# Performance work log

Measured on AMD Instinct MI355X. Metric: run time of the kernel, lower is better.

## Reference

```python
import jax, jax.numpy as jnp
import numpy as np

ARITY = 4
DEPTH = 8          # leaves = ARITY**DEPTH = 65536; internal nodes = (4**8-1)//3 = 21845
IN_DIM = 64
MEM = 128
HID = 128


def setup_inputs() -> dict:
    key = jax.random.key(0)
    ks = jax.random.split(key, 20)
    n_leaves = ARITY ** DEPTH
    n_internal = (ARITY ** DEPTH - 1) // (ARITY - 1)
    s = 0.05
    inp = {
        "inputs": jax.random.normal(ks[0], (n_leaves, IN_DIM), jnp.float32),
        "ops": jax.random.randint(ks[1], (n_internal,), 0, 2, jnp.int32),
        # MLP (all bias-free); torch Linear weight layout [out, in]
        "W1": jax.random.normal(ks[2], (MEM, IN_DIM), jnp.float32) * s,
        "W2": jax.random.normal(ks[3], (3 * MEM, MEM), jnp.float32) * s,
        "W3": jax.random.normal(ks[4], (2 * MEM, 3 * MEM), jnp.float32) * s,
        "Wp": jax.random.normal(ks[5], (MEM, 2 * MEM), jnp.float32) * s,
        # ChildSumTreeRNN
        "Wand": jax.random.normal(ks[6], (MEM, MEM), jnp.float32) * s,
        "Wor": jax.random.normal(ks[7], (MEM, MEM), jnp.float32) * s,
        "Rw1": jax.random.normal(ks[8], (HID, MEM), jnp.float32) * s,
        "Rb1": jnp.zeros((HID,), jnp.float32),
        "Rw2": jax.random.normal(ks[9], (HID, HID), jnp.float32) * s,
        "Rb2": jnp.zeros((HID,), jnp.float32),
        "Rw3": jax.random.normal(ks[10], (HID, HID), jnp.float32) * s,
        "Rb3": jnp.zeros((HID,), jnp.float32),
        "Rwp": jax.random.normal(ks[11], (1, HID), jnp.float32) * s,
        "Rbp": jnp.zeros((1,), jnp.float32),
    }
    return inp


def reference(inputs, ops, W1, W2, W3, Wp, Wand, Wor,
              Rw1, Rb1, Rw2, Rb2, Rw3, Rb3, Rwp, Rbp):
    # MLP embedding of all leaves  [n_leaves, MEM]
    h = jnp.tanh(inputs @ W1.T)
    h = jnp.tanh(h @ W2.T)
    h = jnp.tanh(h @ W3.T)
    h = jnp.tanh(h @ Wp.T)

    # ChildSumTreeRNN, level by level (children before parents).
    # Complete arity-4 tree: level l has 4**l internal nodes; ops is
    # level-ordered from the root, so level l starts at (4**l - 1)//3.
    for l in range(DEPTH - 1, -1, -1):
        n = ARITY ** l
        start = (ARITY ** l - 1) // (ARITY - 1)
        ops_l = ops[start:start + n]                      # [n]
        ch = h.reshape(n, ARITY, MEM)                     # children states
        ha = jnp.tanh(jnp.einsum('ncm,om->nco', ch, Wand)).mean(axis=1)
        ho = jnp.tanh(jnp.einsum('ncm,om->nco', ch, Wor)).mean(axis=1)
        h = jnp.where((ops_l == 0)[:, None], ha, ho)      # [n, MEM]

    x = jax.nn.relu(h @ Rw1.T + Rb1)
    x = jax.nn.relu(x @ Rw2.T + Rb2)
    x = jax.nn.relu(x @ Rw3.T + Rb3)
    out = x @ Rwp.T + Rbp                                 # [1, 1]
    return out
```

## Files before the change

### kernel.cpp

```cpp
#include <hip/hip_runtime.h>
#include <hip/hip_bf16.h>
#include <stdint.h>

#define N_LEAVES 65536
#define MEM 128
#define HID 128

typedef float  f32x4 __attribute__((ext_vector_type(4)));
typedef short  s16x8 __attribute__((ext_vector_type(8)));
typedef unsigned short u16;
typedef u16    u16x8 __attribute__((ext_vector_type(8)));

__device__ __forceinline__ u16 f2bf(float x) {
    unsigned u = __builtin_bit_cast(unsigned, x);
    u += 0x7FFFu + ((u >> 16) & 1u);
    return (u16)(u >> 16);
}
__device__ __forceinline__ float bf2f(u16 b) {
    unsigned u = ((unsigned)b) << 16;
    return __builtin_bit_cast(float, u);
}
__device__ __forceinline__ float hif(float x) {
    return __builtin_bit_cast(float, __builtin_bit_cast(unsigned, x) & 0xffff0000u);
}
__device__ __forceinline__ unsigned packbf(float e0, float e1) {
    return __builtin_amdgcn_perm(__builtin_bit_cast(unsigned, e1),
                                 __builtin_bit_cast(unsigned, e0), 0x07060302u);
}
__device__ __forceinline__ float tanh_c(float x) {
    float E = __builtin_amdgcn_exp2f(x * 2.8853900817779268f);
    return 1.0f - 2.0f * __builtin_amdgcn_rcpf(E + 1.0f);
}
__device__ __forceinline__ float tanh_p(float x) {
    float x2 = x * x;
    float poly = x * (1.0f + x2 * (-0.33333334f + x2 * 0.13333334f));
    float E = __builtin_amdgcn_exp2f(x * 2.8853900817779268f);
    float ex = 1.0f - 2.0f * __builtin_amdgcn_rcpf(E + 1.0f);
    return (__builtin_fabsf(x) < 0.25f) ? poly : ex;
}

__device__ __forceinline__ f32x4 mfma_bf(s16x8 a, s16x8 b, f32x4 c) {
    return __builtin_amdgcn_mfma_f32_16x16x32_bf16(a, b, c, 0, 0, 0);
}

__global__ __launch_bounds__(256) void prep_all(
    const float* __restrict__ W1, const float* __restrict__ W2,
    const float* __restrict__ W3, const float* __restrict__ Wp,
    const float* __restrict__ Wand, const float* __restrict__ Wor,
    u16* __restrict__ w1tH, u16* __restrict__ w1tL,
    u16* __restrict__ w2tH, u16* __restrict__ w2tL,
    u16* __restrict__ w3tH, u16* __restrict__ w3tL,
    u16* __restrict__ wptH, u16* __restrict__ wptL,
    u16* __restrict__ waH,  u16* __restrict__ waL,
    u16* __restrict__ woH,  u16* __restrict__ woL)
{
    int g = blockIdx.x * 256 + threadIdx.x;
    const float* W; u16 *Th, *Tl; int K, N, base;
    if (g < 1024)       { W = W1;  Th = w1tH; Tl = w1tL; N = 128; K = 64;  base = 0; }
    else if (g < 7168)  { W = W2;  Th = w2tH; Tl = w2tL; N = 384; K = 128; base = 1024; }
    else if (g < 19456) { W = W3;  Th = w3tH; Tl = w3tL; N = 256; K = 384; base = 7168; }
    else if (g < 23552) { W = Wp;  Th = wptH; Tl = wptL; N = 128; K = 256; base = 19456; }
    else if (g < 25600) { W = Wand; Th = waH; Tl = waL;  N = 128; K = 128; base = 23552; }
    else if (g < 27648) { W = Wor;  Th = woH; Tl = woL;  N = 128; K = 128; base = 25600; }
    else return;
    int t = g - base;
    int kg8 = K >> 3;
    int n = t / kg8, kg = t - n * kg8;
    const float* src = &W[(size_t)n * K + kg * 8];
    size_t dst = ((size_t)kg * N + n) * 8;
    u16x8 hv, lv;
    #pragma unroll
    for (int j = 0; j < 8; ++j) {
        float v = src[j];
        u16 hb = f2bf(v);
        hv[j] = hb;
        lv[j] = f2bf(v - bf2f(hb));
    }
    *(u16x8*)&Th[dst] = hv;
    *(u16x8*)&Tl[dst] = lv;
}

__device__ __forceinline__ int act_g(int Wu, int row, int c4) {
    return row * (Wu >> 3) + (c4 ^ (row & 7));
}

template<int FJ, int KTN, int WIN, int WOUT>
__device__ __forceinline__ void mlp_layer_t(
    const u16* inH, const u16* inL,
    const u16* __restrict__ BtH, const u16* __restrict__ BtL,
    u16* outH, u16* outL,
    int w, int l)
{
    const int lr = l & 15, lc = l >> 4;
    const int featBase = w * (FJ * 16);
    constexpr int D = (KTN < 3) ? KTN : 3;

    f32x4 acc[FJ][4] = {};
    s16x8 wh[D][FJ], wl[D][FJ];
    s16x8 ah[2][4], al[2][4];

    #pragma unroll
    for (int d = 0; d < D; ++d)
        #pragma unroll
        for (int fi = 0; fi < FJ; ++fi) {
            int o = ((d * 4 + lc) * WOUT + featBase + fi * 16 + lr) * 8;
            wh[d][fi] = *(const s16x8*)&BtH[o];
            wl[d][fi] = *(const s16x8*)&BtL[o];
        }
    #pragma unroll
    for (int rj = 0; rj < 4; ++rj) {
        int off = act_g(WIN, rj * 16 + lr, lc) * 8;
        ah[0][rj] = *(const s16x8*)&inH[off];
        al[0][rj] = *(const s16x8*)&inL[off];
    }

    #pragma unroll
    for (int kt = 0; kt < KTN; ++kt) {
        const int ws_ = kt % D;
        const int as_ = kt & 1;
        if (kt + 1 < KTN) {
            #pragma unroll
            for (int rj = 0; rj < 4; ++rj) {
                int off = act_g(WIN, rj * 16 + lr, (kt + 1) * 4 + lc) * 8;
                ah[as_ ^ 1][rj] = *(const s16x8*)&inH[off];
                al[as_ ^ 1][rj] = *(const s16x8*)&inL[off];
            }
        }
        #pragma unroll
        for (int fi = 0; fi < FJ; ++fi)
            #pragma unroll
            for (int rj = 0; rj < 4; ++rj) {
                f32x4 a = acc[fi][rj];
                a = mfma_bf(wh[ws_][fi], ah[as_][rj], a);
                a = mfma_bf(wh[ws_][fi], al[as_][rj], a);
                a = mfma_bf(wl[ws_][fi], ah[as_][rj], a);
                acc[fi][rj] = a;
            }
        if (kt + D < KTN) {
            #pragma unroll
            for (int fi = 0; fi < FJ; ++fi) {
                int o = (((kt + D) * 4 + lc) * WOUT + featBase + fi * 16 + lr) * 8;
                wh[ws_][fi] = *(const s16x8*)&BtH[o];
                wl[ws_][fi] = *(const s16x8*)&BtL[o];
            }
        }
    }

    #pragma unroll
    for (int fi = 0; fi < FJ; ++fi)
        #pragma unroll
        for (int rj = 0; rj < 4; ++rj) {
            int m  = rj * 16 + lr;
            int n0 = featBase + fi * 16 + lc * 4;
            f32x4 v = acc[fi][rj];
            float t0 = tanh_c(v[0]), t1 = tanh_c(v[1]);
            float t2 = tanh_c(v[2]), t3 = tanh_c(v[3]);
            uint2 hp, lp;
            hp.x = packbf(t0, t1);
            hp.y = packbf(t2, t3);
            lp.x = packbf(t0 - hif(t0), t1 - hif(t1));
            lp.y = packbf(t2 - hif(t2), t3 - hif(t3));
            int go = act_g(WOUT, m, n0 >> 3) * 8 + (n0 & 7);
            *(uint2*)&outH[go] = hp;
            *(uint2*)&outL[go] = lp;
        }
}

template<int CJ, int FJ, bool TOGLOBAL>
__device__ __forceinline__ void tree_level(
    const u16* inH, const u16* inL,
    const u16* __restrict__ wAH, const u16* __restrict__ wAL,
    const u16* __restrict__ wOH, const u16* __restrict__ wOL,
    const int* __restrict__ opsL,
    u16* outH, u16* outL,
    int outRowBase, int nValid, int cfBase, int ffBase, int l)
{
    const int lr = l & 15, lc = l >> 4;
    f32x4 accA[CJ][FJ] = {};
    f32x4 accO[CJ][FJ] = {};

    #pragma unroll
    for (int kt = 0; kt < 4; ++kt) {
        s16x8 ah[CJ], al[CJ];
        #pragma unroll
        for (int c = 0; c < CJ; ++c) {
            int off = act_g(128, (cfBase + c) * 16 + lr, kt * 4 + lc) * 8;
            ah[c] = *(const s16x8*)&inH[off];
            al[c] = *(const s16x8*)&inL[off];
        }
        #pragma unroll
        for (int f = 0; f < FJ; ++f) {
            int wo = ((kt * 4 + lc) * 128 + ffBase + f * 16 + lr) * 8;
            s16x8 bah = *(const s16x8*)&wAH[wo];
            s16x8 bal = *(const s16x8*)&wAL[wo];
            s16x8 boh = *(const s16x8*)&wOH[wo];
            s16x8 bol = *(const s16x8*)&wOL[wo];
            #pragma unroll
            for (int c = 0; c < CJ; ++c) {
                f32x4 a = accA[c][f];
                a = mfma_bf(ah[c], bah, a);
                a = mfma_bf(ah[c], bal, a);
                a = mfma_bf(al[c], bah, a);
                accA[c][f] = a;
                f32x4 o = accO[c][f];
                o = mfma_bf(ah[c], boh, o);
                o = mfma_bf(ah[c], bol, o);
                o = mfma_bf(al[c], boh, o);
                accO[c][f] = o;
            }
        }
    }

    #pragma unroll
    for (int c = 0; c < CJ; ++c) {
        int p = (cfBase + c) * 4 + lc;
        if (p < nValid) {
            int op = opsL[p];
            #pragma unroll
            for (int f = 0; f < FJ; ++f) {
                f32x4 v = op ? accO[c][f] : accA[c][f];
                float t = 0.25f * (tanh_p(v[0]) + tanh_p(v[1]) + tanh_p(v[2]) + tanh_p(v[3]));
                unsigned bits = __builtin_bit_cast(unsigned, t);
                u16 hb = (u16)(bits >> 16);
                float lof = t - __builtin_bit_cast(float, bits & 0xffff0000u);
                u16 lb = (u16)(__builtin_bit_cast(unsigned, lof) >> 16);
                int feat = ffBase + f * 16 + lr;
                if constexpr (TOGLOBAL) {
                    int ga = (outRowBase + p) * 128 + feat;
                    outH[ga] = hb;
                    outL[ga] = lb;
                } else {
                    int go = act_g(128, outRowBase + p, feat >> 3) * 8 + (feat & 7);
                    outH[go] = hb;
                    outL[go] = lb;
                }
            }
        }
    }
}

__global__ __launch_bounds__(512, 1) void leaf_fused(
    const float* __restrict__ x,
    const u16* __restrict__ W1tH, const u16* __restrict__ W1tL,
    const u16* __restrict__ W2tH, const u16* __restrict__ W2tL,
    const u16* __restrict__ W3tH, const u16* __restrict__ W3tL,
    const u16* __restrict__ WptH, const u16* __restrict__ WptL,
    const u16* __restrict__ waH,  const u16* __restrict__ waL,
    const u16* __restrict__ woH,  const u16* __restrict__ woL,
    const int* __restrict__ ops,
    u16* __restrict__ l7H, u16* __restrict__ l7L)
{
    __shared__ u16 bufA[49152];
    __shared__ u16 bufB[32768];

    const int tid = threadIdx.x;
    const int w = tid >> 6, l = tid & 63;
    const int blk = blockIdx.x;
    const int rowBase = blk * 64;

    {
        int row = tid >> 3;
        int c0  = (tid & 7) * 8;
        const float* src = &x[(size_t)(rowBase + row) * 64 + c0];
        float4 v0 = *(const float4*)src;
        float4 v1 = *(const float4*)(src + 4);
        float xs[8] = {v0.x, v0.y, v0.z, v0.w, v1.x, v1.y, v1.z, v1.w};
        int go = act_g(64, row, c0 >> 3) * 8;
        uint4 hp, lp;
        hp.x = packbf(xs[0], xs[1]); hp.y = packbf(xs[2], xs[3]);
        hp.z = packbf(xs[4], xs[5]); hp.w = packbf(xs[6], xs[7]);
        lp.x = packbf(xs[0] - hif(xs[0]), xs[1] - hif(xs[1]));
        lp.y = packbf(xs[2] - hif(xs[2]), xs[3] - hif(xs[3]));
        lp.z = packbf(xs[4] - hif(xs[4]), xs[5] - hif(xs[5]));
        lp.w = packbf(xs[6] - hif(xs[6]), xs[7] - hif(xs[7]));
        *(uint4*)&bufB[go] = hp;
        *(uint4*)&bufB[4096 + go] = lp;
    }
    __syncthreads();

    mlp_layer_t<1, 2, 64, 128>(bufB, bufB + 4096, W1tH, W1tL,
                               bufB + 8192, bufB + 16384, w, l);
    __syncthreads();
    mlp_layer_t<3, 4, 128, 384>(bufB + 8192, bufB + 16384, W2tH, W2tL,
                                bufA, bufA + 24576, w, l);
    __syncthreads();
    mlp_layer_t<2, 12, 384, 256>(bufA, bufA + 24576, W3tH, W3tL,
                                 bufB, bufB + 16384, w, l);
    __syncthreads();
    mlp_layer_t<1, 8, 256, 128>(bufB, bufB + 16384, WptH, WptL,
                                bufA, bufA + 8192, w, l);
    __syncthreads();
    tree_level<1, 4, true>(bufA, bufA + 8192, waH, waL, woH, woL,
                           ops + 5461 + blk * 16, l7H, l7L,
                           blk * 16, 16, (w >> 1), (w & 1) * 64, l);
}

__global__ __launch_bounds__(512, 4) void tree3(
    const u16* __restrict__ inH, const u16* __restrict__ inL,
    const u16* __restrict__ wAH, const u16* __restrict__ wAL,
    const u16* __restrict__ wOH, const u16* __restrict__ wOL,
    const int* __restrict__ ops0, const int* __restrict__ ops1,
    const int* __restrict__ ops2,
    u16* __restrict__ outH, u16* __restrict__ outL)
{
    __shared__ u16 L0H[16384], L0L[16384];
    __shared__ u16 L1H[4096],  L1L[4096];

    const int tid = threadIdx.x;
    const int w = tid >> 6, l = tid & 63;
    const int blk = blockIdx.x;

    #pragma unroll
    for (int it = 0; it < 4; ++it) {
        int g = tid + it * 512;
        int row = g >> 4, c4 = g & 15;
        size_t src = (size_t)(blk * 128 + row) * 128 + c4 * 8;
        int dst = act_g(128, row, c4) * 8;
        *(u16x8*)&L0H[dst] = *(const u16x8*)&inH[src];
        *(u16x8*)&L0L[dst] = *(const u16x8*)&inL[src];
    }
    __syncthreads();

    tree_level<2, 4, false>(L0H, L0L, wAH, wAL, wOH, wOL, ops0 + blk * 32,
                            L1H, L1L, 0, 32, (w & 3) * 2, (w >> 2) * 64, l);
    __syncthreads();
    tree_level<1, 2, false>(L1H, L1L, wAH, wAL, wOH, wOL, ops1 + blk * 8,
                            L0H, L0L, 0, 8, (w >> 2), (w & 3) * 32, l);
    __syncthreads();
    tree_level<1, 1, true>(L0H, L0L, wAH, wAL, wOH, wOL, ops2 + blk * 2,
                           outH, outL, blk * 2, 2, 0, w * 16, l);
}

__global__ __launch_bounds__(128) void tail_final(
    const u16* __restrict__ l1H, const u16* __restrict__ l1L,
    const int* __restrict__ ops,
    const float* __restrict__ Wand, const float* __restrict__ Wor,
    const float* __restrict__ Rw1, const float* __restrict__ Rb1,
    const float* __restrict__ Rw2, const float* __restrict__ Rb2,
    const float* __restrict__ Rw3, const float* __restrict__ Rb3,
    const float* __restrict__ Rwp, const float* __restrict__ Rbp,
    float* __restrict__ out)
{
    __shared__ float h[512];
    __shared__ float F[512];
    const int o = threadIdx.x;

    for (int i = o; i < 512; i += 128) h[i] = bf2f(l1H[i]) + bf2f(l1L[i]);
    __syncthreads();

    {
        const float* Wsel = (ops[0] == 0) ? Wand : Wor;
        const float4* wr = (const float4*)&Wsel[o * 128];
        const float4* h0 = (const float4*)&h[0];
        const float4* h1 = (const float4*)&h[128];
        const float4* h2 = (const float4*)&h[256];
        const float4* h3 = (const float4*)&h[384];
        float s0 = 0, s1 = 0, s2 = 0, s3 = 0;
        for (int m = 0; m < 32; ++m) {
            float4 wv = wr[m];
            float4 a0 = h0[m], a1 = h1[m], a2 = h2[m], a3 = h3[m];
            s0 += wv.x*a0.x + wv.y*a0.y + wv.z*a0.z + wv.w*a0.w;
            s1 += wv.x*a1.x + wv.y*a1.y + wv.z*a1.z + wv.w*a1.w;
            s2 += wv.x*a2.x + wv.y*a2.y + wv.z*a2.z + wv.w*a2.w;
            s3 += wv.x*a3.x + wv.y*a3.y + wv.z*a3.z + wv.w*a3.w;
        }
        F[o] = 0.25f * (tanh_p(s0) + tanh_p(s1) + tanh_p(s2) + tanh_p(s3));
    }
    __syncthreads();
    {
        const float4* wr = (const float4*)&Rw1[o * 128];
        const float4* xr = (const float4*)&F[0];
        float s = 0;
        for (int m = 0; m < 32; ++m) {
            float4 wv = wr[m], xv = xr[m];
            s += wv.x*xv.x + wv.y*xv.y + wv.z*xv.z + wv.w*xv.w;
        }
        __syncthreads();
        F[128 + o] = fmaxf(s + Rb1[o], 0.f);
    }
    __syncthreads();
    {
        const float4* wr = (const float4*)&Rw2[o * 128];
        const float4* xr = (const float4*)&F[128];
        float s = 0;
        for (int m = 0; m < 32; ++m) {
            float4 wv = wr[m], xv = xr[m];
            s += wv.x*xv.x + wv.y*xv.y + wv.z*xv.z + wv.w*xv.w;
        }
        __syncthreads();
        F[256 + o] = fmaxf(s + Rb2[o], 0.f);
    }
    __syncthreads();
    {
        const float4* wr = (const float4*)&Rw3[o * 128];
        const float4* xr = (const float4*)&F[256];
        float s = 0;
        for (int m = 0; m < 32; ++m) {
            float4 wv = wr[m], xv = xr[m];
            s += wv.x*xv.x + wv.y*xv.y + wv.z*xv.z + wv.w*xv.w;
        }
        __syncthreads();
        F[384 + o] = fmaxf(s + Rb3[o], 0.f) * Rwp[o];
    }
    __syncthreads();
    if (o == 0) {
        float t = 0.f;
        for (int i = 0; i < 128; ++i) t += F[384 + i];
        out[0] = t + Rbp[0];
    }
}

extern "C" void kernel_launch(void* const* d_in, const int* in_sizes, int n_in,
                              void* d_out, int out_size, void* d_ws, size_t ws_size,
                              hipStream_t stream)
{
    const float* inputs = (const float*)d_in[0];
    const int*   ops    = (const int*)d_in[1];
    const float* W1     = (const float*)d_in[2];
    const float* W2     = (const float*)d_in[3];
    const float* W3     = (const float*)d_in[4];
    const float* Wp     = (const float*)d_in[5];
    const float* Wand   = (const float*)d_in[6];
    const float* Wor    = (const float*)d_in[7];
    const float* Rw1    = (const float*)d_in[8];
    const float* Rb1    = (const float*)d_in[9];
    const float* Rw2    = (const float*)d_in[10];
    const float* Rb2    = (const float*)d_in[11];
    const float* Rw3    = (const float*)d_in[12];
    const float* Rb3    = (const float*)d_in[13];
    const float* Rwp    = (const float*)d_in[14];
    const float* Rbp    = (const float*)d_in[15];
    float* out = (float*)d_out;
    u16* ws = (u16*)d_ws;

    size_t off = 0;
    u16* w1tH = ws + off; off += 8192;   u16* w1tL = ws + off; off += 8192;
    u16* w2tH = ws + off; off += 49152;  u16* w2tL = ws + off; off += 49152;
    u16* w3tH = ws + off; off += 98304;  u16* w3tL = ws + off; off += 98304;
    u16* wptH = ws + off; off += 32768;  u16* wptL = ws + off; off += 32768;
    u16* waH  = ws + off; off += 16384;  u16* waL  = ws + off; off += 16384;
    u16* woH  = ws + off; off += 16384;  u16* woL  = ws + off; off += 16384;
    u16* l7H  = ws + off; off += (size_t)16384 * 128;
    u16* l7L  = ws + off; off += (size_t)16384 * 128;
    u16* l4H  = ws + off; off += 256 * 128;
    u16* l4L  = ws + off; off += 256 * 128;
    u16* l1H  = ws + off; off += 512;
    u16* l1L  = ws + off; off += 512;

    prep_all<<<108, 256, 0, stream>>>(W1, W2, W3, Wp, Wand, Wor,
        w1tH, w1tL, w2tH, w2tL, w3tH, w3tL, wptH, wptL, waH, waL, woH, woL);

    leaf_fused<<<N_LEAVES / 64, 512, 0, stream>>>(
        inputs, w1tH, w1tL, w2tH, w2tL, w3tH, w3tL, wptH, wptL,
        waH, waL, woH, woL, ops, l7H, l7L);

    tree3<<<128, 512, 0, stream>>>(l7H, l7L, waH, waL, woH, woL,
        ops + 1365, ops + 341, ops + 85, l4H, l4L);

    tree3<<<2, 512, 0, stream>>>(l4H, l4L, waH, waL, woH, woL,
        ops + 21, ops + 5, ops + 1, l1H, l1L);

    tail_final<<<1, 128, 0, stream>>>(l1H, l1L, ops, Wand, Wor,
        Rw1, Rb1, Rw2, Rb2, Rw3, Rb3, Rwp, Rbp, out);
}
```

Measured before the change: 143.0 us.

## Chunk W2/W3 layers to shrink LDS footprint and raise leaf kernel occupancy

The fused leaf MLP kernel now computes the 384-wide hidden layer in three 128-wide chunks, each immediately consumed by a partial K-slice of the W3 layer, so the full 384-wide activation never sits in shared memory. LDS drops from two buffers (~160KB) to one 64KB pool with aliased regions, and launch bounds go from 1 to 4 blocks per CU. The MFMA inner loop is restructured to double-buffer weights and load activations per row tile instead of double-buffering activations. This adds extra barriers and register pressure from the 4-block bound, but aims to hide latency through more resident waves.

```diff
diff --git a/kernel.cpp b/kernel.cpp
--- a/kernel.cpp
+++ b/kernel.cpp
@@ -84,68 +84,56 @@
     return row * (Wu >> 3) + (c4 ^ (row & 7));
 }
 
-template<int FJ, int KTN, int WIN, int WOUT>
-__device__ __forceinline__ void mlp_layer_t(
+template<int FJ, int KTN, int WINU, int WSTR>
+__device__ __forceinline__ void mlp_core(
+    f32x4 (&acc)[FJ][4],
     const u16* inH, const u16* inL,
     const u16* __restrict__ BtH, const u16* __restrict__ BtL,
-    u16* outH, u16* outL,
-    int w, int l)
+    int kt0, int featBase, int l)
 {
     const int lr = l & 15, lc = l >> 4;
-    const int featBase = w * (FJ * 16);
-    constexpr int D = (KTN < 3) ? KTN : 3;
-
-    f32x4 acc[FJ][4] = {};
-    s16x8 wh[D][FJ], wl[D][FJ];
-    s16x8 ah[2][4], al[2][4];
-
-    #pragma unroll
-    for (int d = 0; d < D; ++d)
-        #pragma unroll
-        for (int fi = 0; fi < FJ; ++fi) {
-            int o = ((d * 4 + lc) * WOUT + featBase + fi * 16 + lr) * 8;
-            wh[d][fi] = *(const s16x8*)&BtH[o];
-            wl[d][fi] = *(const s16x8*)&BtL[o];
-        }
-    #pragma unroll
-    for (int rj = 0; rj < 4; ++rj) {
-        int off = act_g(WIN, rj * 16 + lr, lc) * 8;
-        ah[0][rj] = *(const s16x8*)&inH[off];
-        al[0][rj] = *(const s16x8*)&inL[off];
+    s16x8 wh[2][FJ], wl[2][FJ];
+
+    #pragma unroll
+    for (int fi = 0; fi < FJ; ++fi) {
+        int o = ((kt0 * 4 + lc) * WSTR + featBase + fi * 16 + lr) * 8;
+        wh[0][fi] = *(const s16x8*)&BtH[o];
+        wl[0][fi] = *(const s16x8*)&BtL[o];
     }
 
     #pragma unroll
     for (int kt = 0; kt < KTN; ++kt) {
-        const int ws_ = kt % D;
-        const int as_ = kt & 1;
+        const int cur = kt & 1;
         if (kt + 1 < KTN) {
             #pragma unroll
-            for (int rj = 0; rj < 4; ++rj) {
-                int off = act_g(WIN, rj * 16 + lr, (kt + 1) * 4 + lc) * 8;
-                ah[as_ ^ 1][rj] = *(const s16x8*)&inH[off];
-                al[as_ ^ 1][rj] = *(const s16x8*)&inL[off];
+            for (int fi = 0; fi < FJ; ++fi) {
+                int o = (((kt0 + kt + 1) * 4 + lc) * WSTR + featBase + fi * 16 + lr) * 8;
+                wh[cur ^ 1][fi] = *(const s16x8*)&BtH[o];
+                wl[cur ^ 1][fi] = *(const s16x8*)&BtL[o];
             }
         }
         #pragma unroll
-        for (int fi = 0; fi < FJ; ++fi)
+        for (int rj = 0; rj < 4; ++rj) {
+            int off = act_g(WINU, rj * 16 + lr, kt * 4 + lc) * 8;
+            s16x8 ah = *(const s16x8*)&inH[off];
+            s16x8 al = *(const s16x8*)&inL[off];
             #pragma unroll
-            for (int rj = 0; rj < 4; ++rj) {
+            for (int fi = 0; fi < FJ; ++fi) {
                 f32x4 a = acc[fi][rj];
-                a = mfma_bf(wh[ws_][fi], ah[as_][rj], a);
-                a = mfma_bf(wh[ws_][fi], al[as_][rj], a);
-                a = mfma_bf(wl[ws_][fi], ah[as_][rj], a);
+                a = mfma_bf(wh[cur][fi], ah, a);
+                a = mfma_bf(wh[cur][fi], al, a);
+                a = mfma_bf(wl[cur][fi], ah, a);
                 acc[fi][rj] = a;
             }
-        if (kt + D < KTN) {
-            #pragma unroll
-            for (int fi = 0; fi < FJ; ++fi) {
-                int o = (((kt + D) * 4 + lc) * WOUT + featBase + fi * 16 + lr) * 8;
-                wh[ws_][fi] = *(const s16x8*)&BtH[o];
-                wl[ws_][fi] = *(const s16x8*)&BtL[o];
-            }
-        }
-    }
-
+        }
+    }
+}
+
+template<int FJ, int WOUTU>
+__device__ __forceinline__ void write_act(
+    f32x4 (&acc)[FJ][4], u16* outH, u16* outL, int featBase, int l)
+{
+    const int lr = l & 15, lc = l >> 4;
     #pragma unroll
     for (int fi = 0; fi < FJ; ++fi)
         #pragma unroll
@@ -160,7 +148,7 @@
             hp.y = packbf(t2, t3);
             lp.x = packbf(t0 - hif(t0), t1 - hif(t1));
             lp.y = packbf(t2 - hif(t2), t3 - hif(t3));
-            int go = act_g(WOUT, m, n0 >> 3) * 8 + (n0 & 7);
+            int go = act_g(WOUTU, m, n0 >> 3) * 8 + (n0 & 7);
             *(uint2*)&outH[go] = hp;
             *(uint2*)&outL[go] = lp;
         }
@@ -239,7 +227,7 @@
     }
 }
 
-__global__ __launch_bounds__(512, 1) void leaf_fused(
+__global__ __launch_bounds__(512, 4) void leaf_fused(
     const float* __restrict__ x,
     const u16* __restrict__ W1tH, const u16* __restrict__ W1tL,
     const u16* __restrict__ W2tH, const u16* __restrict__ W2tL,
@@ -250,8 +238,13 @@
     const int* __restrict__ ops,
     u16* __restrict__ l7H, u16* __restrict__ l7L)
 {
-    __shared__ u16 bufA[49152];
-    __shared__ u16 bufB[32768];
+    __shared__ u16 pool[32768];
+
+    u16* h1H = pool;               u16* h1L = pool + 8192;
+    u16* xH  = pool + 16384;       u16* xL  = pool + 20480;
+    u16* h2H = pool + 16384;       u16* h2L = pool + 24576;
+    u16* h3H = pool;               u16* h3L = pool + 16384;
+    u16* h4H = pool;               u16* h4L = pool + 8192;
 
     const int tid = threadIdx.x;
     const int w = tid >> 6, l = tid & 63;
@@ -273,24 +266,44 @@
         lp.y = packbf(xs[2] - hif(xs[2]), xs[3] - hif(xs[3]));
         lp.z = packbf(xs[4] - hif(xs[4]), xs[5] - hif(xs[5]));
         lp.w = packbf(xs[6] - hif(xs[6]), xs[7] - hif(xs[7]));
-        *(uint4*)&bufB[go] = hp;
-        *(uint4*)&bufB[4096 + go] = lp;
-    }
-    __syncthreads();
-
-    mlp_layer_t<1, 2, 64, 128>(bufB, bufB + 4096, W1tH, W1tL,
-                               bufB + 8192, bufB + 16384, w, l);
-    __syncthreads();
-    mlp_layer_t<3, 4, 128, 384>(bufB + 8192, bufB + 16384, W2tH, W2tL,
-                                bufA, bufA + 24576, w, l);
-    __syncthreads();
-    mlp_layer_t<2, 12, 384, 256>(bufA, bufA + 24576, W3tH, W3tL,
-                                 bufB, bufB + 16384, w, l);
-    __syncthreads();
-    mlp_layer_t<1, 8, 256, 128>(bufB, bufB + 16384, WptH, WptL,
-                                bufA, bufA + 8192, w, l);
-    __syncthreads();
-    tree_level<1, 4, true>(bufA, bufA + 8192, waH, waL, woH, woL,
+        *(uint4*)&xH[go] = hp;
+        *(uint4*)&xL[go] = lp;
+    }
+    __syncthreads();
+
+    {
+        f32x4 acc1[1][4] = {};
+        mlp_core<1, 2, 64, 128>(acc1, xH, xL, W1tH, W1tL, 0, w * 16, l);
+        write_act<1, 128>(acc1, h1H, h1L, w * 16, l);
+    }
+    __syncthreads();
+
+    f32x4 acc3[2][4] = {};
+    #pragma unroll
+    for (int p = 0; p < 3; ++p) {
+        if (p) __syncthreads();
+        {
+            f32x4 acc2[1][4] = {};
+            mlp_core<1, 4, 128, 384>(acc2, h1H, h1L, W2tH, W2tL, 0,
+                                     p * 128 + w * 16, l);
+            write_act<1, 128>(acc2, h2H, h2L, w * 16, l);
+        }
+        __syncthreads();
+        mlp_core<2, 4, 128, 256>(acc3, h2H, h2L, W3tH, W3tL, p * 4, w * 32, l);
+    }
+    __syncthreads();
+    write_act<2, 256>(acc3, h3H, h3L, w * 32, l);
+    __syncthreads();
+
+    {
+        f32x4 acc4[1][4] = {};
+        mlp_core<1, 8, 256, 128>(acc4, h3H, h3L, WptH, WptL, 0, w * 16, l);
+        __syncthreads();
+        write_act<1, 128>(acc4, h4H, h4L, w * 16, l);
+    }
+    __syncthreads();
+
+    tree_level<1, 4, true>(h4H, h4L, waH, waL, woH, woL,
                            ops + 5461 + blk * 16, l7H, l7L,
                            blk * 16, 16, (w >> 1), (w & 1) * 64, l);
 }
```

New measurement: 133.9 us (median of 2 runs). 6.3% less time.
